# Kernel tuning notes

Hardware: AMD Instinct MI355X
Metric: run time of the kernel (lower is better)

Reference implementation:

```python
import jax, jax.numpy as jnp
import numpy as np
import math

B, T, D = 2, 2048, 1024
H, HS = 16, 64  # n_heads, head_size; D == H*HS


def setup_inputs() -> dict:
    key = jax.random.key(0)
    k1, k2, k3 = jax.random.split(key, 3)
    x = jax.random.normal(k1, (B, T, D), dtype=jnp.float32)
    w_qkv = jax.random.normal(k2, (D, 3 * D), dtype=jnp.float32) * (1.0 / math.sqrt(D))
    b_qkv = jnp.zeros((3 * D,), dtype=jnp.float32)
    w_out = jax.random.normal(k3, (D, D), dtype=jnp.float32) * (1.0 / math.sqrt(D))
    b_out = jnp.zeros((D,), dtype=jnp.float32)
    return {"x": x, "w_qkv": w_qkv, "b_qkv": b_qkv, "w_out": w_out, "b_out": b_out}


def reference(x, w_qkv, b_qkv, w_out, b_out):
    b, t, d = x.shape
    qkv = x @ w_qkv + b_qkv                       # (B,T,3D)
    q, k, v = jnp.split(qkv, 3, axis=-1)
    # (B,T,D) -> (B,H,T,HS)
    q = q.reshape(b, t, H, HS).transpose(0, 2, 1, 3)
    k = k.reshape(b, t, H, HS).transpose(0, 2, 1, 3)
    v = v.reshape(b, t, H, HS).transpose(0, 2, 1, 3)
    scale = 1.0 / math.sqrt(HS)
    attn = jnp.einsum('bhqd,bhkd->bhqk', q, k) * scale  # (B,H,T,T)
    causal = jnp.tril(jnp.ones((t, t), dtype=bool))
    attn = jnp.where(causal[None, None], attn, -jnp.inf)
    attn = jax.nn.softmax(attn, axis=-1)
    o = jnp.einsum('bhqk,bhkd->bhqd', attn, v)          # (B,H,T,HS)
    o = o.transpose(0, 2, 1, 3).reshape(b, t, d)
    return o @ w_out + b_out
```

## Files before the change

kernel.cpp:

```cpp
#include <hip/hip_runtime.h>
#include <math.h>

#define B_  2
#define T_  2048
#define D_  1024
#define H_  16
#define HS_ 64
#define M_  (B_*T_)

typedef __bf16 bf16x8 __attribute__((ext_vector_type(8)));
typedef float  f32x4  __attribute__((ext_vector_type(4)));
typedef unsigned short u16;

static __device__ __forceinline__ u16 f2bf(float f) {
    unsigned int u = __float_as_uint(f);
    u += 0x7fff + ((u >> 16) & 1);
    return (u16)(u >> 16);
}

static __device__ __forceinline__ void glds16(const u16* g, u16* l) {
    __builtin_amdgcn_global_load_lds(
        (const __attribute__((address_space(1))) void*)g,
        (__attribute__((address_space(3))) void*)l, 16, 0, 0);
}

__global__ void cast_kernel(const float* __restrict__ in, u16* __restrict__ out) {
    int i = (blockIdx.x * blockDim.x + threadIdx.x) * 4;
    float4 v = *reinterpret_cast<const float4*>(in + i);
    ushort4 o;
    o.x = f2bf(v.x); o.y = f2bf(v.y); o.z = f2bf(v.z); o.w = f2bf(v.w);
    *reinterpret_cast<ushort4*>(out + i) = o;
}

__global__ void transpose_cast(const float* __restrict__ in, u16* __restrict__ out,
                               int R, int C) {
    __shared__ float tile[32][33];
    int c0 = blockIdx.x * 32, r0 = blockIdx.y * 32;
    int tx = threadIdx.x, ty = threadIdx.y;
    #pragma unroll
    for (int j = 0; j < 4; ++j)
        tile[ty + j*8][tx] = in[(size_t)(r0 + ty + j*8) * C + c0 + tx];
    __syncthreads();
    #pragma unroll
    for (int j = 0; j < 4; ++j)
        out[(size_t)(c0 + ty + j*8) * R + r0 + tx] = f2bf(tile[tx][ty + j*8]);
}

template<int MODE>
__global__ __launch_bounds__(256) void gemm_bt(
    const u16* __restrict__ A, const u16* __restrict__ Bt,
    const float* __restrict__ bias,
    float* __restrict__ Cf,
    u16* __restrict__ Qb, u16* __restrict__ Kb, u16* __restrict__ Vt,
    int M, int N, int K)
{
    __shared__ u16 As[128][32];
    __shared__ u16 Bs[128][32];
    int tid  = threadIdx.x;
    int lane = tid & 63, wave = tid >> 6;
    int wm = wave >> 1, wn = wave & 1;
    int quad = lane >> 4, lr = lane & 15;
    int bm = blockIdx.x, bn = blockIdx.y;

    f32x4 acc[4][4] = {};

    const u16* Ab = A  + (size_t)(bm * 128) * K;
    const u16* Bb = Bt + (size_t)(bn * 128) * K;

    int r0 = tid >> 2,           c0 = (tid & 3) * 8;
    int r1 = (tid + 256) >> 2,   c1 = ((tid + 256) & 3) * 8;

    for (int k0 = 0; k0 < K; k0 += 32) {
        __syncthreads();
        glds16(Ab + (size_t)r0 * K + k0 + c0, &As[r0][c0]);
        glds16(Ab + (size_t)r1 * K + k0 + c1, &As[r1][c1]);
        glds16(Bb + (size_t)r0 * K + k0 + c0, &Bs[r0][c0]);
        glds16(Bb + (size_t)r1 * K + k0 + c1, &Bs[r1][c1]);
        __syncthreads();
        bf16x8 af[4], bfr[4];
        #pragma unroll
        for (int i = 0; i < 4; ++i)
            af[i] = *reinterpret_cast<const bf16x8*>(&As[wm*64 + i*16 + lr][quad*8]);
        #pragma unroll
        for (int j = 0; j < 4; ++j)
            bfr[j] = *reinterpret_cast<const bf16x8*>(&Bs[wn*64 + j*16 + lr][quad*8]);
        #pragma unroll
        for (int i = 0; i < 4; ++i)
            #pragma unroll
            for (int j = 0; j < 4; ++j)
                acc[i][j] = __builtin_amdgcn_mfma_f32_16x16x32_bf16(af[i], bfr[j], acc[i][j], 0, 0, 0);
    }

    #pragma unroll
    for (int i = 0; i < 4; ++i) {
        int mrow = bm*128 + wm*64 + i*16 + quad*4;
        #pragma unroll
        for (int j = 0; j < 4; ++j) {
            int ncol = bn*128 + wn*64 + j*16 + lr;
            float bv = bias[ncol];
            #pragma unroll
            for (int r = 0; r < 4; ++r) {
                float v = acc[i][j][r] + bv;
                int m = mrow + r;
                if (MODE == 1) {
                    Cf[(size_t)m * N + ncol] = v;
                } else {
                    int b = m >> 11, t = m & (T_ - 1);
                    int s = ncol >> 10, rem = ncol & 1023;
                    int h = rem >> 6, d = rem & 63;
                    int bh = b * H_ + h;
                    if (s == 0)      Qb[((size_t)bh*T_ + t)*HS_ + d] = f2bf(v * 0.125f);
                    else if (s == 1) Kb[((size_t)bh*T_ + t)*HS_ + d] = f2bf(v);
                    else             Vt[((size_t)bh*HS_ + d)*T_ + t] = f2bf(v);
                }
            }
        }
    }
}

__global__ __launch_bounds__(512) void attn_kernel(
    const u16* __restrict__ Qb, const u16* __restrict__ Kb,
    const u16* __restrict__ Vt, u16* __restrict__ Ob)
{
    __shared__ u16 Ks[64][72];
    __shared__ u16 Vs[64][72];
    __shared__ u16 Ps[8][16][72];

    int tid  = threadIdx.x;
    int lane = tid & 63, wave = tid >> 6;
    int quad = lane >> 4, lr = lane & 15;

    int lin = blockIdx.x;
    int bh  = (lin & 7) + 8 * ((lin >> 3) & 3);
    int p   = lin >> 5;

    int grp   = wave >> 2;
    int myqt  = grp ? (31 - p) : p;
    int jdiag = myqt;
    int jmax  = 31 - p;
    int qw    = myqt * 64 + (wave & 3) * 16;

    const u16* Qp = Qb + ((size_t)bh * T_ + qw) * HS_;
    bf16x8 qf[2];
    #pragma unroll
    for (int h2 = 0; h2 < 2; ++h2)
        qf[h2] = *reinterpret_cast<const bf16x8*>(Qp + lr*HS_ + h2*32 + quad*8);

    f32x4 Oa[4] = {};
    float lrow[4] = {0.f, 0.f, 0.f, 0.f};

    int srow = tid >> 3, scol = (tid & 7) * 8;
    const u16* Kst = Kb + ((size_t)bh*T_ + srow)*HS_ + scol;
    const u16* Vst = Vt + ((size_t)bh*HS_ + srow)*T_ + scol;

    bf16x8 kpre = *reinterpret_cast<const bf16x8*>(Kst);
    bf16x8 vpre = *reinterpret_cast<const bf16x8*>(Vst);

    for (int jt = 0; jt <= jmax; ++jt) {
        __syncthreads();
        *reinterpret_cast<bf16x8*>(&Ks[srow][scol]) = kpre;
        *reinterpret_cast<bf16x8*>(&Vs[srow][scol]) = vpre;
        if (jt < jmax) {
            int kn = (jt + 1) * 64;
            kpre = *reinterpret_cast<const bf16x8*>(Kst + (size_t)kn * HS_);
            vpre = *reinterpret_cast<const bf16x8*>(Vst + kn);
        }
        __syncthreads();

        if (jt <= jdiag) {
            int kb = jt * 64;
            f32x4 Sa[4];
            #pragma unroll
            for (int nt = 0; nt < 4; ++nt) {
                f32x4 z = {};
                bf16x8 b0 = *reinterpret_cast<const bf16x8*>(&Ks[nt*16 + lr][quad*8]);
                bf16x8 b1 = *reinterpret_cast<const bf16x8*>(&Ks[nt*16 + lr][32 + quad*8]);
                z = __builtin_amdgcn_mfma_f32_16x16x32_bf16(qf[0], b0, z, 0, 0, 0);
                z = __builtin_amdgcn_mfma_f32_16x16x32_bf16(qf[1], b1, z, 0, 0, 0);
                Sa[nt] = z;
            }

            if (jt == jdiag) {
                #pragma unroll
                for (int nt = 0; nt < 4; ++nt)
                    #pragma unroll
                    for (int r = 0; r < 4; ++r) {
                        int kg = kb + nt*16 + lr;
                        int qg = qw + quad*4 + r;
                        if (kg > qg) Sa[nt][r] = -INFINITY;
                    }
            }

            #pragma unroll
            for (int nt = 0; nt < 4; ++nt)
                #pragma unroll
                for (int r = 0; r < 4; ++r) {
                    float pv = __expf(Sa[nt][r]);
                    lrow[r] += pv;
                    Ps[wave][quad*4 + r][nt*16 + lr] = f2bf(pv);
                }

            #pragma unroll
            for (int kk = 0; kk < 2; ++kk) {
                bf16x8 pa = *reinterpret_cast<const bf16x8*>(&Ps[wave][lr][kk*32 + quad*8]);
                #pragma unroll
                for (int nt = 0; nt < 4; ++nt) {
                    bf16x8 vb = *reinterpret_cast<const bf16x8*>(&Vs[nt*16 + lr][kk*32 + quad*8]);
                    Oa[nt] = __builtin_amdgcn_mfma_f32_16x16x32_bf16(pa, vb, Oa[nt], 0, 0, 0);
                }
            }
        }
    }

    int b = bh >> 4, h = bh & 15;
    #pragma unroll
    for (int r = 0; r < 4; ++r) {
        float s = lrow[r];
        #pragma unroll
        for (int off = 8; off >= 1; off >>= 1)
            s += __shfl_xor(s, off, 64);
        float inv = 1.f / s;
        int qg = qw + quad*4 + r;
        #pragma unroll
        for (int nt = 0; nt < 4; ++nt) {
            int d = nt*16 + lr;
            Ob[((size_t)b*T_ + qg)*D_ + h*HS_ + d] = f2bf(Oa[nt][r] * inv);
        }
    }
}

extern "C" void kernel_launch(void* const* d_in, const int* in_sizes, int n_in,
                              void* d_out, int out_size, void* d_ws, size_t ws_size,
                              hipStream_t stream) {
    (void)in_sizes; (void)n_in; (void)out_size; (void)ws_size;
    const float* x     = (const float*)d_in[0];
    const float* w_qkv = (const float*)d_in[1];
    const float* b_qkv = (const float*)d_in[2];
    const float* w_out = (const float*)d_in[3];
    const float* b_out = (const float*)d_in[4];
    float* out = (float*)d_out;

    char* ws = (char*)d_ws;
    u16* Xb    = (u16*)ws; ws += (size_t)M_ * D_ * 2;
    u16* WqkvT = (u16*)ws; ws += (size_t)3 * D_ * D_ * 2;
    u16* WoutT = (u16*)ws; ws += (size_t)D_ * D_ * 2;
    u16* Qb    = (u16*)ws; ws += (size_t)M_ * D_ * 2;
    u16* Kb    = (u16*)ws; ws += (size_t)M_ * D_ * 2;
    u16* Vt    = (u16*)ws; ws += (size_t)M_ * D_ * 2;
    u16* Ob    = (u16*)ws; ws += (size_t)M_ * D_ * 2;

    cast_kernel<<<M_ * D_ / 1024, 256, 0, stream>>>(x, Xb);
    transpose_cast<<<dim3(3*D_/32, D_/32), dim3(32, 8), 0, stream>>>(w_qkv, WqkvT, D_, 3*D_);
    transpose_cast<<<dim3(D_/32,   D_/32), dim3(32, 8), 0, stream>>>(w_out, WoutT, D_, D_);
    gemm_bt<0><<<dim3(M_/128, 3*D_/128), 256, 0, stream>>>(
        Xb, WqkvT, b_qkv, nullptr, Qb, Kb, Vt, M_, 3*D_, D_);
    attn_kernel<<<512, 512, 0, stream>>>(Qb, Kb, Vt, Ob);
    gemm_bt<1><<<dim3(M_/128, D_/128), 256, 0, stream>>>(
        Ob, WoutT, b_out, out, nullptr, nullptr, nullptr, M_, D_, D_);
}
```

Baseline: 191.9 us.

## Fuse prep kernels, swizzle GEMM LDS layout, reorder attention block schedule

Merges the activation cast and both weight transpose-casts into one launch that uses vectorized float4 loads and ushort4 stores. The GEMM shared-memory tiles get an XOR swizzle on 16-byte chunks to cut bank conflicts on the MFMA fragment reads. The attention grid mapping is reversed for the second half of the blocks so heavy and light causal tiles are interleaved differently across launch order. This removes two launches and aims to reduce LDS conflicts and tail imbalance, at the cost of more index arithmetic.

```diff
diff --git a/kernel.cpp b/kernel.cpp
--- a/kernel.cpp
+++ b/kernel.cpp
@@ -24,26 +24,44 @@
         (__attribute__((address_space(3))) void*)l, 16, 0, 0);
 }
 
-__global__ void cast_kernel(const float* __restrict__ in, u16* __restrict__ out) {
-    int i = (blockIdx.x * blockDim.x + threadIdx.x) * 4;
-    float4 v = *reinterpret_cast<const float4*>(in + i);
+static __device__ __forceinline__ bf16x8 lds_chunk4(const u16* base, int row, int c) {
+    return *reinterpret_cast<const bf16x8*>(base + (size_t)(row * 4 + (c ^ ((row >> 1) & 3))) * 8);
+}
+
+__global__ __launch_bounds__(256) void prep_kernel(
+    const float* __restrict__ x, const float* __restrict__ w_qkv,
+    const float* __restrict__ w_out,
+    u16* __restrict__ Xb, u16* __restrict__ WqkvT, u16* __restrict__ WoutT)
+{
+    int bid = blockIdx.x;
+    if (bid < 4096) {
+        int i = (bid * 256 + threadIdx.x) * 4;
+        float4 v = *reinterpret_cast<const float4*>(x + i);
+        ushort4 o;
+        o.x = f2bf(v.x); o.y = f2bf(v.y); o.z = f2bf(v.z); o.w = f2bf(v.w);
+        *reinterpret_cast<ushort4*>(Xb + i) = o;
+        return;
+    }
+    const float* in; u16* out; int C; int c0, r0;
+    if (bid < 4096 + 3072) {
+        int t = bid - 4096;
+        in = w_qkv; out = WqkvT; C = 3 * D_;
+        c0 = (t % 96) * 32; r0 = (t / 96) * 32;
+    } else {
+        int t = bid - 7168;
+        in = w_out; out = WoutT; C = D_;
+        c0 = (t & 31) * 32; r0 = (t >> 5) * 32;
+    }
+    __shared__ float tile[32][33];
+    int tr = threadIdx.x >> 3, tc4 = (threadIdx.x & 7) * 4;
+    float4 v = *reinterpret_cast<const float4*>(in + (size_t)(r0 + tr) * C + c0 + tc4);
+    tile[tr][tc4+0] = v.x; tile[tr][tc4+1] = v.y;
+    tile[tr][tc4+2] = v.z; tile[tr][tc4+3] = v.w;
+    __syncthreads();
     ushort4 o;
-    o.x = f2bf(v.x); o.y = f2bf(v.y); o.z = f2bf(v.z); o.w = f2bf(v.w);
-    *reinterpret_cast<ushort4*>(out + i) = o;
-}
-
-__global__ void transpose_cast(const float* __restrict__ in, u16* __restrict__ out,
-                               int R, int C) {
-    __shared__ float tile[32][33];
-    int c0 = blockIdx.x * 32, r0 = blockIdx.y * 32;
-    int tx = threadIdx.x, ty = threadIdx.y;
-    #pragma unroll
-    for (int j = 0; j < 4; ++j)
-        tile[ty + j*8][tx] = in[(size_t)(r0 + ty + j*8) * C + c0 + tx];
-    __syncthreads();
-    #pragma unroll
-    for (int j = 0; j < 4; ++j)
-        out[(size_t)(c0 + ty + j*8) * R + r0 + tx] = f2bf(tile[tx][ty + j*8]);
+    o.x = f2bf(tile[tc4+0][tr]); o.y = f2bf(tile[tc4+1][tr]);
+    o.z = f2bf(tile[tc4+2][tr]); o.w = f2bf(tile[tc4+3][tr]);
+    *reinterpret_cast<ushort4*>(out + (size_t)(c0 + tr) * D_ + r0 + tc4) = o;
 }
 
 template<int MODE>
@@ -54,8 +72,8 @@
     u16* __restrict__ Qb, u16* __restrict__ Kb, u16* __restrict__ Vt,
     int M, int N, int K)
 {
-    __shared__ u16 As[128][32];
-    __shared__ u16 Bs[128][32];
+    __shared__ u16 As[128 * 32];
+    __shared__ u16 Bs[128 * 32];
     int tid  = threadIdx.x;
     int lane = tid & 63, wave = tid >> 6;
     int wm = wave >> 1, wn = wave & 1;
@@ -67,23 +85,23 @@
     const u16* Ab = A  + (size_t)(bm * 128) * K;
     const u16* Bb = Bt + (size_t)(bn * 128) * K;
 
-    int r0 = tid >> 2,           c0 = (tid & 3) * 8;
-    int r1 = (tid + 256) >> 2,   c1 = ((tid + 256) & 3) * 8;
+    int r0 = tid >> 2,         c0 = (((tid) & 3) ^ ((tid >> 3) & 3)) * 8;
+    int r1 = (tid + 256) >> 2, c1 = (((tid + 256) & 3) ^ (((tid + 256) >> 3) & 3)) * 8;
 
     for (int k0 = 0; k0 < K; k0 += 32) {
         __syncthreads();
-        glds16(Ab + (size_t)r0 * K + k0 + c0, &As[r0][c0]);
-        glds16(Ab + (size_t)r1 * K + k0 + c1, &As[r1][c1]);
-        glds16(Bb + (size_t)r0 * K + k0 + c0, &Bs[r0][c0]);
-        glds16(Bb + (size_t)r1 * K + k0 + c1, &Bs[r1][c1]);
+        glds16(Ab + (size_t)r0 * K + k0 + c0, As + (size_t)tid * 8);
+        glds16(Ab + (size_t)r1 * K + k0 + c1, As + (size_t)(tid + 256) * 8);
+        glds16(Bb + (size_t)r0 * K + k0 + c0, Bs + (size_t)tid * 8);
+        glds16(Bb + (size_t)r1 * K + k0 + c1, Bs + (size_t)(tid + 256) * 8);
         __syncthreads();
         bf16x8 af[4], bfr[4];
         #pragma unroll
         for (int i = 0; i < 4; ++i)
-            af[i] = *reinterpret_cast<const bf16x8*>(&As[wm*64 + i*16 + lr][quad*8]);
+            af[i] = lds_chunk4(As, wm*64 + i*16 + lr, quad);
         #pragma unroll
         for (int j = 0; j < 4; ++j)
-            bfr[j] = *reinterpret_cast<const bf16x8*>(&Bs[wn*64 + j*16 + lr][quad*8]);
+            bfr[j] = lds_chunk4(Bs, wn*64 + j*16 + lr, quad);
         #pragma unroll
         for (int i = 0; i < 4; ++i)
             #pragma unroll
@@ -130,9 +148,12 @@
     int lane = tid & 63, wave = tid >> 6;
     int quad = lane >> 4, lr = lane & 15;
 
-    int lin = blockIdx.x;
-    int bh  = (lin & 7) + 8 * ((lin >> 3) & 3);
-    int p   = lin >> 5;
+    int lin  = blockIdx.x;
+    int l2   = lin & 255;
+    int half = lin >> 8;
+    int pp   = l2 >> 5;
+    int p    = half ? (15 - pp) : pp;
+    int bh   = (l2 & 7) + 8 * ((l2 >> 3) & 3);
 
     int grp   = wave >> 2;
     int myqt  = grp ? (31 - p) : p;
@@ -161,8 +182,8 @@
         *reinterpret_cast<bf16x8*>(&Ks[srow][scol]) = kpre;
         *reinterpret_cast<bf16x8*>(&Vs[srow][scol]) = vpre;
         if (jt < jmax) {
-            int kn = (jt + 1) * 64;
-            kpre = *reinterpret_cast<const bf16x8*>(Kst + (size_t)kn * HS_);
+            size_t kn = (size_t)(jt + 1) * 64;
+            kpre = *reinterpret_cast<const bf16x8*>(Kst + kn * HS_);
             vpre = *reinterpret_cast<const bf16x8*>(Vst + kn);
         }
         __syncthreads();
@@ -249,9 +270,7 @@
     u16* Vt    = (u16*)ws; ws += (size_t)M_ * D_ * 2;
     u16* Ob    = (u16*)ws; ws += (size_t)M_ * D_ * 2;
 
-    cast_kernel<<<M_ * D_ / 1024, 256, 0, stream>>>(x, Xb);
-    transpose_cast<<<dim3(3*D_/32, D_/32), dim3(32, 8), 0, stream>>>(w_qkv, WqkvT, D_, 3*D_);
-    transpose_cast<<<dim3(D_/32,   D_/32), dim3(32, 8), 0, stream>>>(w_out, WoutT, D_, D_);
+    prep_kernel<<<8192, 256, 0, stream>>>(x, w_qkv, w_out, Xb, WqkvT, WoutT);
     gemm_bt<0><<<dim3(M_/128, 3*D_/128), 256, 0, stream>>>(
         Xb, WqkvT, b_qkv, nullptr, Qb, Kb, Vt, M_, 3*D_, D_);
     attn_kernel<<<512, 512, 0, stream>>>(Qb, Kb, Vt, Ob);
```

New measurement: 189.4 us. Within noise of the previous version (-1.3%).
